# Kernel optimization log

Hardware: AMD Instinct MI355X
Metric: run time of the kernel (lower is better)

## Reference

```python
import jax, jax.numpy as jnp
import numpy as np
from jax import lax

P = 16        # patch spatial size (C = 3 * P * P = 768)
CH = 3        # channels per patch
H = 8         # num attention heads
EPS_BN = 1e-3 # keras BatchNormalization default epsilon
EPS_LN = 1e-3 # keras LayerNormalization default epsilon


def _layernorm(x, g, b):
    mu = jnp.mean(x, axis=-1, keepdims=True)
    var = jnp.mean(jnp.square(x - mu), axis=-1, keepdims=True)
    return (x - mu) * lax.rsqrt(var + EPS_LN) * g + b


def setup_inputs() -> dict:
    key = jax.random.key(0)
    ks = jax.random.split(key, 8)
    B, N, C, DFF = 8, 1024, 768, 3072
    s = 0.02
    return {
        "encoded_patches": jax.random.normal(ks[0], (B, N, C), jnp.float32),
        "qconv_w": jax.random.normal(ks[1], (3, 3, CH, CH), jnp.float32) * 0.2,
        "reatten_w": jax.random.normal(ks[2], (H, H), jnp.float32) * 0.3,
        "reatten_b": jnp.zeros((H,), jnp.float32),
        "bn_gamma": jnp.ones((H,), jnp.float32),
        "bn_beta": jnp.zeros((H,), jnp.float32),
        "proj_w": jax.random.normal(ks[3], (C, C), jnp.float32) * s,
        "proj_b": jnp.zeros((C,), jnp.float32),
        "ffn_w1": jax.random.normal(ks[4], (C, DFF), jnp.float32) * s,
        "ffn_b1": jnp.zeros((DFF,), jnp.float32),
        "ffn_w2": jax.random.normal(ks[5], (DFF, C), jnp.float32) * s,
        "ffn_b2": jnp.zeros((C,), jnp.float32),
        "ln1_g": jnp.ones((C,), jnp.float32),
        "ln1_b": jnp.zeros((C,), jnp.float32),
        "ln2_g": jnp.ones((C,), jnp.float32),
        "ln2_b": jnp.zeros((C,), jnp.float32),
    }


def reference(encoded_patches, qconv_w, reatten_w, reatten_b, bn_gamma, bn_beta,
              proj_w, proj_b, ffn_w1, ffn_b1, ffn_w2, ffn_b2,
              ln1_g, ln1_b, ln2_g, ln2_b):
    B, N, C = encoded_patches.shape
    hd = C // H
    scale = jnp.float32(hd) ** -0.5

    # create_queries: unflatten [B,N,C] -> [B*N,P,P,CH], 3x3 'same' conv,
    # flatten back and split heads -> [B,H,N,hd]. Source uses qconv2d for
    # q, k AND v, so q == k == v; compute once.
    y = encoded_patches.reshape(B * N, P, P, CH)
    y = lax.conv_general_dilated(y, qconv_w, (1, 1), 'SAME',
                                 dimension_numbers=('NHWC', 'HWIO', 'NHWC'))
    q = y.reshape(B, N, H, hd).transpose(0, 2, 1, 3)  # [B,H,N,hd]
    k = q
    v = q

    # attention scores + softmax: [B,H,N,N]
    attn = jax.nn.softmax(jnp.einsum('bhnd,bhmd->bhnm', q, k) * scale, axis=-1)

    # re-attention: 1x1 conv mixing heads + BatchNorm (inference: mean=0, var=1)
    attn = jnp.einsum('bhnm,gh->bgnm', attn, reatten_w) + reatten_b[None, :, None, None]
    bn_s = bn_gamma * lax.rsqrt(jnp.float32(1.0) + EPS_BN)
    attn = attn * bn_s[None, :, None, None] + bn_beta[None, :, None, None]
    # reatten_scale = 1.0 (transform_scale=False)

    x = jnp.einsum('bhnm,bhmd->bhnd', attn, v)        # [B,H,N,hd]
    x = x.transpose(0, 2, 1, 3).reshape(B, N, C)
    x = x @ proj_w + proj_b

    x = x + encoded_patches          # residual
    x = _layernorm(x, ln1_g, ln1_b)  # LN1

    h = jax.nn.gelu(x @ ffn_w1 + ffn_b1, approximate=False)
    x = (h @ ffn_w2 + ffn_b2) + x    # FFN + residual
    x = _layernorm(x, ln2_g, ln2_b)  # LN2
    return x
```

## Files before the change

kernel.cpp:

```cpp
#include <hip/hip_runtime.h>
#include <hip/hip_bf16.h>
#include <math.h>

#define B_ 8
#define N_ 1024
#define C_ 768
#define H_ 8
#define HD_ 96
#define DFF_ 3072
#define SC2_ 0.14724454f
#define SH2_ 11.5415602f

typedef __attribute__((ext_vector_type(8))) short bf16x8;
typedef __attribute__((ext_vector_type(4))) float f32x4;
typedef __attribute__((ext_vector_type(4))) short sh4;

__device__ __forceinline__ short f2bf(float f){
  __hip_bfloat16 h = __float2bfloat16(f);
  return __builtin_bit_cast(short, h);
}
__device__ __forceinline__ float bf2f(short s){
  unsigned u = ((unsigned)(unsigned short)s) << 16;
  return __builtin_bit_cast(float, u);
}
#define MFMA16(a,b,c) __builtin_amdgcn_mfma_f32_16x16x32_bf16((a),(b),(c),0,0,0)

__device__ __forceinline__ void gload16(const void* g, void* l){
  __builtin_amdgcn_global_load_lds((const __attribute__((address_space(1))) unsigned int*)g,
                                   (__attribute__((address_space(3))) unsigned int*)l, 16, 0, 0);
}

__global__ void conv_q_kernel(const float* __restrict__ x, const float* __restrict__ w,
                              short* __restrict__ qb){
  int p = blockIdx.x;
  int t = threadIdx.x;
  __shared__ float xs[768];
  __shared__ float ws[81];
  const float* xp = x + (size_t)p * 768;
  xs[t] = xp[t]; xs[t+256] = xp[t+256]; xs[t+512] = xp[t+512];
  if (t < 81) ws[t] = w[t];
  __syncthreads();
  int i = t >> 4, j = t & 15;
  float a0=0.f, a1=0.f, a2=0.f;
  #pragma unroll
  for (int di=0; di<3; ++di){
    int ii = i + di - 1;
    if (ii < 0 || ii > 15) continue;
    #pragma unroll
    for (int dj=0; dj<3; ++dj){
      int jj = j + dj - 1;
      if (jj < 0 || jj > 15) continue;
      const float* cell = &xs[(ii*16+jj)*3];
      const float* wp = &ws[(di*3+dj)*9];
      #pragma unroll
      for (int ci=0; ci<3; ++ci){
        float xv = cell[ci];
        a0 += xv * wp[ci*3+0];
        a1 += xv * wp[ci*3+1];
        a2 += xv * wp[ci*3+2];
      }
    }
  }
  short* qp = qb + (size_t)p*768 + t*3;
  qp[0]=f2bf(a0); qp[1]=f2bf(a1); qp[2]=f2bf(a2);
}

__global__ void vt_kernel(const short* __restrict__ in, short* __restrict__ out){
  __shared__ short tile[32][33];
  int b = blockIdx.z;
  int c0 = blockIdx.x*32, n0 = blockIdx.y*32;
  int t = threadIdx.x;
  const short* ib = in + (size_t)b*N_*C_;
  short* ob = out + (size_t)b*C_*N_;
  #pragma unroll
  for (int i=0;i<4;i++){
    int idx = i*256+t; int r = idx>>5, cc = idx&31;
    tile[r][cc] = ib[(size_t)(n0+r)*C_ + c0+cc];
  }
  __syncthreads();
  #pragma unroll
  for (int i=0;i<4;i++){
    int idx = i*256+t; int r = idx>>5, cc = idx&31;
    ob[(size_t)(c0+r)*N_ + n0+cc] = tile[cc][r];
  }
}

__global__ void wtrans_kernel(const float* __restrict__ in, short* __restrict__ out,
                              int K, int Nn){
  __shared__ float tile[32][33];
  int n0 = blockIdx.x*32, k0 = blockIdx.y*32;
  int t = threadIdx.x;
  #pragma unroll
  for (int i=0;i<4;i++){
    int idx=i*256+t; int r=idx>>5, cc=idx&31;
    tile[r][cc] = in[(size_t)(k0+r)*Nn + n0+cc];
  }
  __syncthreads();
  #pragma unroll
  for (int i=0;i<4;i++){
    int idx=i*256+t; int r=idx>>5, cc=idx&31;
    out[(size_t)(n0+r)*K + k0+cc] = f2bf(tile[cc][r]);
  }
}

__global__ __launch_bounds__(256, 2)
void qkexp_kernel(const short* __restrict__ qb, short* __restrict__ Pt,
                  float* __restrict__ lsums, int b0)
{
  __shared__ short Ks[64*104];
  int bid = blockIdx.x;
  int bhl = bid >> 4, nt = bid & 15;
  int b = b0 + (bhl >> 3), h = bhl & 7;
  int n0 = nt*64;
  int t = threadIdx.x, w = t>>6, l = t&63, lg = l>>4, lr = l&15;
  const short* qbase = qb + (size_t)b*N_*C_;

  bf16x8 qf[3];
  #pragma unroll
  for (int kc=0;kc<3;++kc)
    qf[kc] = *(const bf16x8*)(qbase + (size_t)(n0 + w*16 + lr)*C_ + h*HD_ + kc*32 + lg*8);

  bf16x8 kreg[3];
  #pragma unroll
  for (int i=0;i<3;++i){
    int id = i*256+t; int r = id/12, c = id%12;
    kreg[i] = *(const bf16x8*)(qbase + (size_t)r*C_ + h*HD_ + c*8);
  }

  float lsum = 0.f;
  short* prow = Pt + ((size_t)bhl*1024 + n0 + w*16 + lr)*1024;

  for (int mt=0; mt<16; ++mt){
    int m0 = mt*64;
    __syncthreads();
    #pragma unroll
    for (int i=0;i<3;++i){
      int id = i*256+t; int r = id/12, c = id%12;
      *(bf16x8*)&Ks[r*104 + c*8] = kreg[i];
    }
    __syncthreads();
    if (mt < 15){
      int m1 = m0 + 64;
      #pragma unroll
      for (int i=0;i<3;++i){
        int id = i*256+t; int r = id/12, c = id%12;
        kreg[i] = *(const bf16x8*)(qbase + (size_t)(m1+r)*C_ + h*HD_ + c*8);
      }
    }
    #pragma unroll
    for (int s=0;s<4;++s){
      f32x4 sacc = (f32x4){0.f,0.f,0.f,0.f};
      bf16x8 kf[3];
      #pragma unroll
      for (int kc=0;kc<3;++kc)
        kf[kc] = *(const bf16x8*)&Ks[(s*16+lr)*104 + kc*32 + lg*8];
      #pragma unroll
      for (int kc=0;kc<3;++kc)
        sacc = MFMA16(kf[kc], qf[kc], sacc);
      sh4 pv;
      #pragma unroll
      for (int r=0;r<4;++r){
        float e = exp2f(sacc[r]*SC2_ - SH2_);
        lsum += e;
        pv[r] = f2bf(e);
      }
      *(sh4*)&prow[m0 + s*16 + lg*4] = pv;
    }
  }
  lsum += __shfl_xor(lsum, 16);
  lsum += __shfl_xor(lsum, 32);
  if (l < 16) lsums[(size_t)bhl*1024 + n0 + w*16 + l] = lsum;
}

__device__ __forceinline__ void load_mix(const short* __restrict__ Pt, int b_local,
                                         int n0, int m0, int t,
                                         const float wl[4][8], float cw, bf16x8 amc[4]){
  #pragma unroll
  for (int i=0;i<4;++i){
    int r = i*32 + (t>>3), mo = t&7;
    const short* p0 = Pt + ((size_t)(b_local*8)*1024 + (size_t)(n0+r))*1024 + m0 + mo*8;
    float pm[8];
    #pragma unroll
    for (int j=0;j<8;++j) pm[j] = cw;
    #pragma unroll
    for (int h=0;h<8;++h){
      bf16x8 ph = *(const bf16x8*)(p0 + (size_t)h*1024*1024);
      #pragma unroll
      for (int j=0;j<8;++j) pm[j] += wl[i][h]*bf2f(ph[j]);
    }
    #pragma unroll
    for (int j=0;j<8;++j) amc[i][j] = f2bf(pm[j]);
  }
}

__global__ __launch_bounds__(256, 2)
void mixpv_kernel(const short* __restrict__ Pt, const float* __restrict__ lsums,
                  const short* __restrict__ vt, const float* __restrict__ rw,
                  const float* __restrict__ rb, const float* __restrict__ bng,
                  const float* __restrict__ bnb, short* __restrict__ out, int b0)
{
  __shared__ short Am[128*68];
  int bid = blockIdx.x;
  int rank = bid>>3;
  int g = rank & 7;
  int p = (bid&7) + ((rank>>3)<<3);
  int b_local = p>>3;
  int n0 = (p&7)*128;
  int b = b0 + b_local;
  int t = threadIdx.x, w = t>>6, l = t&63, lg = l>>4, lr = l&15;

  float bns = bng[g]*rsqrtf(1.001f);
  float cw = rb[g]*bns + bnb[g];
  float wl[4][8];
  #pragma unroll
  for (int i=0;i<4;++i){
    int r = i*32 + (t>>3);
    #pragma unroll
    for (int h=0;h<8;++h)
      wl[i][h] = (rw[g*8+h]*bns) / lsums[(size_t)(b_local*8+h)*1024 + n0 + r];
  }

  f32x4 acc[2][6];
  #pragma unroll
  for (int a=0;a<2;++a)
    #pragma unroll
    for (int nt=0;nt<6;++nt) acc[a][nt] = (f32x4){0.f,0.f,0.f,0.f};

  bf16x8 amc[4];
  load_mix(Pt, b_local, n0, 0, t, wl, cw, amc);
  const short* vbase = vt + (size_t)b*C_*N_ + (size_t)g*HD_*N_;

  for (int mt=0; mt<16; ++mt){
    int m0 = mt*64;
    __syncthreads();
    #pragma unroll
    for (int i=0;i<4;++i){
      int r = i*32 + (t>>3), mo = t&7;
      *(bf16x8*)&Am[r*68 + mo*8] = amc[i];
    }
    __syncthreads();
    if (mt < 15) load_mix(Pt, b_local, n0, m0+64, t, wl, cw, amc);
    #pragma unroll
    for (int kc=0;kc<2;++kc){
      bf16x8 af[2], bfr[6];
      #pragma unroll
      for (int a=0;a<2;++a)
        af[a] = *(const bf16x8*)&Am[(w*32 + a*16 + lr)*68 + kc*32 + lg*8];
      #pragma unroll
      for (int nt=0;nt<6;++nt)
        bfr[nt] = *(const bf16x8*)(vbase + (size_t)(nt*16+lr)*N_ + m0 + kc*32 + lg*8);
      #pragma unroll
      for (int a=0;a<2;++a)
        #pragma unroll
        for (int nt=0;nt<6;++nt)
          acc[a][nt] = MFMA16(af[a], bfr[nt], acc[a][nt]);
    }
  }

  short* obase = out + (size_t)b*N_*C_;
  #pragma unroll
  for (int a=0;a<2;++a)
    #pragma unroll
    for (int nt=0;nt<6;++nt)
      #pragma unroll
      for (int r=0;r<4;++r)
        obase[(size_t)(n0 + w*32 + a*16 + lg*4 + r)*C_ + g*HD_ + nt*16 + lr]
            = f2bf(acc[a][nt][r]);
}

template<int EPI>
__global__ __launch_bounds__(256, 2)
void gemm_bt_kernel(const short* __restrict__ A, const short* __restrict__ Bt,
                    const float* __restrict__ bias, const float* __restrict__ res,
                    float* __restrict__ Of, short* __restrict__ Ob,
                    int M, int Nn, int K)
{
  __shared__ __align__(16) char smem[65536];
  short* Sb = (short*)smem;
  int gm = blockIdx.y*128, gn = blockIdx.x*128;
  int tid = threadIdx.x;
  int w = tid>>6, l = tid&63, lg = l>>4, lr = l&15;
  int wr = w>>1, wc = w&1;
  int srow = l>>3;
  int sg = (l&7) ^ srow;

  const short* Ap = A  + (size_t)(gm + w*8 + srow)*K + sg*8;
  const short* Bp = Bt + (size_t)(gn + w*8 + srow)*K + sg*8;

  f32x4 acc[4][4];
  #pragma unroll
  for (int mt=0;mt<4;++mt)
    #pragma unroll
    for (int nt=0;nt<4;++nt) acc[mt][nt] = (f32x4){0.f,0.f,0.f,0.f};

  int nk = K >> 6;

  {
    short* dA = Sb; short* dB = Sb + 8192;
    #pragma unroll
    for (int j=0;j<4;++j){
      gload16(Ap + (size_t)j*32*K, dA + (j*32 + w*8)*64);
      gload16(Bp + (size_t)j*32*K, dB + (j*32 + w*8)*64);
    }
  }
  asm volatile("s_waitcnt vmcnt(0)" ::: "memory");
  __syncthreads();

  int cur = 0;
  for (int t=0; t<nk; ++t){
    if (t+1 < nk){
      short* dA = Sb + (cur^1)*16384;
      short* dB = dA + 8192;
      int kb = (t+1)<<6;
      #pragma unroll
      for (int j=0;j<4;++j){
        gload16(Ap + (size_t)j*32*K + kb, dA + (j*32 + w*8)*64);
        gload16(Bp + (size_t)j*32*K + kb, dB + (j*32 + w*8)*64);
      }
    }
    short* CA = Sb + cur*16384;
    short* CB = CA + 8192;
    #pragma unroll
    for (int kc=0;kc<2;++kc){
      bf16x8 af[4], bfr[4];
      #pragma unroll
      for (int mt=0;mt<4;++mt){
        int row = wr*64+mt*16+lr;
        af[mt] = *(const bf16x8*)&CA[row*64 + (((kc*4+lg)^(lr&7))*8)];
      }
      #pragma unroll
      for (int nt=0;nt<4;++nt){
        int row = wc*64+nt*16+lr;
        bfr[nt] = *(const bf16x8*)&CB[row*64 + (((kc*4+lg)^(lr&7))*8)];
      }
      #pragma unroll
      for (int mt=0;mt<4;++mt)
        #pragma unroll
        for (int nt=0;nt<4;++nt)
          acc[mt][nt] = MFMA16(af[mt], bfr[nt], acc[mt][nt]);
    }
    asm volatile("s_waitcnt vmcnt(0)" ::: "memory");
    __syncthreads();
    cur ^= 1;
  }

  float* Cl = (float*)smem;
  #pragma unroll
  for (int mt=0;mt<4;++mt)
    #pragma unroll
    for (int nt=0;nt<4;++nt)
      #pragma unroll
      for (int r=0;r<4;++r){
        int row = wr*64 + mt*16 + lg*4 + r;
        int col = wc*64 + nt*16 + lr;
        Cl[row*128 + (col ^ ((row&7)<<2))] = acc[mt][nt][r];
      }
  __syncthreads();
  #pragma unroll
  for (int seg=0; seg<16; ++seg){
    int row = seg*8 + (tid>>5);
    int col = (tid&31)*4;
    int colp = col ^ ((row&7)<<2);
    f32x4 c = *(f32x4*)&Cl[row*128 + colp];
    float4 bi = *(const float4*)&bias[gn+col];
    size_t goff = (size_t)(gm+row)*Nn + gn + col;
    if (EPI == 0){
      float4 rs = *(const float4*)&res[goff];
      float4 o = { c[0]+bi.x+rs.x, c[1]+bi.y+rs.y, c[2]+bi.z+rs.z, c[3]+bi.w+rs.w };
      *(float4*)&Of[goff] = o;
    } else {
      float v0 = c[0]+bi.x, v1 = c[1]+bi.y, v2 = c[2]+bi.z, v3 = c[3]+bi.w;
      v0 = 0.5f*v0*(1.0f + erff(v0*0.70710678118654752f));
      v1 = 0.5f*v1*(1.0f + erff(v1*0.70710678118654752f));
      v2 = 0.5f*v2*(1.0f + erff(v2*0.70710678118654752f));
      v3 = 0.5f*v3*(1.0f + erff(v3*0.70710678118654752f));
      sh4 ob = { f2bf(v0), f2bf(v1), f2bf(v2), f2bf(v3) };
      *(sh4*)&Ob[goff] = ob;
    }
  }
}

template<int WB>
__global__ void ln_kernel(const float* __restrict__ in, const float* __restrict__ gam,
                          const float* __restrict__ bet, float* __restrict__ of,
                          short* __restrict__ ob)
{
  int row = blockIdx.x*4 + (threadIdx.x>>6);
  int l = threadIdx.x & 63;
  const float* ip = in + (size_t)row*C_;
  float v[12];
  #pragma unroll
  for (int i=0;i<3;i++) *(float4*)&v[i*4] = *(const float4*)(ip + i*256 + l*4);
  float s = 0.f;
  #pragma unroll
  for (int i=0;i<12;i++) s += v[i];
  #pragma unroll
  for (int off=1; off<64; off<<=1) s += __shfl_xor(s, off);
  float mu = s * (1.0f/768.0f);
  float q = 0.f;
  #pragma unroll
  for (int i=0;i<12;i++){ float d = v[i]-mu; q += d*d; }
  #pragma unroll
  for (int off=1; off<64; off<<=1) q += __shfl_xor(q, off);
  float rstd = rsqrtf(q*(1.0f/768.0f) + 1e-3f);
  #pragma unroll
  for (int i=0;i<3;i++){
    float4 gv = *(const float4*)(gam + i*256 + l*4);
    float4 bv = *(const float4*)(bet + i*256 + l*4);
    float o0 = (v[i*4+0]-mu)*rstd*gv.x + bv.x;
    float o1 = (v[i*4+1]-mu)*rstd*gv.y + bv.y;
    float o2 = (v[i*4+2]-mu)*rstd*gv.z + bv.z;
    float o3 = (v[i*4+3]-mu)*rstd*gv.w + bv.w;
    float4 ov = {o0,o1,o2,o3};
    *(float4*)(of + (size_t)row*C_ + i*256 + l*4) = ov;
    if (WB){
      sh4 obv = { f2bf(o0), f2bf(o1), f2bf(o2), f2bf(o3) };
      *(sh4*)(ob + (size_t)row*C_ + i*256 + l*4) = obv;
    }
  }
}

extern "C" void kernel_launch(void* const* d_in, const int* in_sizes, int n_in,
                              void* d_out, int out_size, void* d_ws, size_t ws_size,
                              hipStream_t stream)
{
  const float* enc       = (const float*)d_in[0];
  const float* qconv_w   = (const float*)d_in[1];
  const float* reatten_w = (const float*)d_in[2];
  const float* reatten_b = (const float*)d_in[3];
  const float* bn_gamma  = (const float*)d_in[4];
  const float* bn_beta   = (const float*)d_in[5];
  const float* proj_w    = (const float*)d_in[6];
  const float* proj_b    = (const float*)d_in[7];
  const float* ffn_w1    = (const float*)d_in[8];
  const float* ffn_b1    = (const float*)d_in[9];
  const float* ffn_w2    = (const float*)d_in[10];
  const float* ffn_b2    = (const float*)d_in[11];
  const float* ln1_g     = (const float*)d_in[12];
  const float* ln1_b     = (const float*)d_in[13];
  const float* ln2_g     = (const float*)d_in[14];
  const float* ln2_b     = (const float*)d_in[15];
  float* outp = (float*)d_out;

  char* ws = (char*)d_ws;
  short* qbuf  = (short*)(ws);
  short* vtbuf = (short*)(ws + 12582912);
  short* atbuf = (short*)(ws + 25165824);
  short* ptbuf = (short*)(ws + 37748736);
  float* lsums = (float*)(ws + 104857600);
  float* ypre  = (float*)(ws + 37748736);
  float* x1    = (float*)(ws + 62914560);
  short* x1b   = (short*)(ws + 88080384);
  short* hbuf  = (short*)(ws + 100663296);
  short* wpt   = (short*)(ws + 150994944);
  short* w1t   = (short*)(ws + 152174592);
  short* w2t   = (short*)(ws + 156893184);

  conv_q_kernel<<<B_*N_, 256, 0, stream>>>(enc, qconv_w, qbuf);
  vt_kernel<<<dim3(C_/32, N_/32, B_), 256, 0, stream>>>(qbuf, vtbuf);
  wtrans_kernel<<<dim3(C_/32,  C_/32), 256, 0, stream>>>(proj_w, wpt, C_,  C_);
  wtrans_kernel<<<dim3(DFF_/32, C_/32), 256, 0, stream>>>(ffn_w1, w1t, C_,  DFF_);
  wtrans_kernel<<<dim3(C_/32, DFF_/32), 256, 0, stream>>>(ffn_w2, w2t, DFF_, C_);

  for (int half=0; half<2; ++half){
    int b0 = half*4;
    qkexp_kernel<<<512, 256, 0, stream>>>(qbuf, ptbuf, lsums, b0);
    mixpv_kernel<<<256, 256, 0, stream>>>(ptbuf, lsums, vtbuf, reatten_w, reatten_b,
                                          bn_gamma, bn_beta, atbuf, b0);
  }

  gemm_bt_kernel<0><<<dim3(C_/128, (B_*N_)/128), 256, 0, stream>>>(
      atbuf, wpt, proj_b, enc, ypre, nullptr, B_*N_, C_, C_);
  ln_kernel<1><<<(B_*N_)/4, 256, 0, stream>>>(ypre, ln1_g, ln1_b, x1, x1b);
  gemm_bt_kernel<1><<<dim3(DFF_/128, (B_*N_)/128), 256, 0, stream>>>(
      x1b, w1t, ffn_b1, nullptr, nullptr, hbuf, B_*N_, DFF_, C_);
  gemm_bt_kernel<0><<<dim3(C_/128, (B_*N_)/128), 256, 0, stream>>>(
      hbuf, w2t, ffn_b2, x1, ypre, nullptr, B_*N_, C_, DFF_);
  ln_kernel<0><<<(B_*N_)/4, 256, 0, stream>>>(ypre, ln2_g, ln2_b, outp, nullptr);
}
```

Baseline: 387.0 us.

## Prefetch two K-stages ahead in GEMM with partial vmcnt waits

Restructures the GEMM main loop so two stages of global-to-LDS loads are in flight: the prologue issues stages 0 and 1, and each iteration waits only until the current stage has landed (vmcnt(8)) before computing. After the MFMAs it waits on LDS reads, barriers, and issues stage t+2 into the freed buffer. This is meant to hide more global load latency behind compute, at the cost of an extra barrier per iteration and reliance on exact vmcnt accounting.

```diff
diff --git a/kernel.cpp b/kernel.cpp
--- a/kernel.cpp
+++ b/kernel.cpp
@@ -295,30 +295,25 @@
 
   int nk = K >> 6;
 
-  {
-    short* dA = Sb; short* dB = Sb + 8192;
+  auto stage = [&](int tt){
+    short* dA = Sb + (tt&1)*16384;
+    short* dB = dA + 8192;
+    int kb = tt<<6;
     #pragma unroll
     for (int j=0;j<4;++j){
-      gload16(Ap + (size_t)j*32*K, dA + (j*32 + w*8)*64);
-      gload16(Bp + (size_t)j*32*K, dB + (j*32 + w*8)*64);
-    }
-  }
-  asm volatile("s_waitcnt vmcnt(0)" ::: "memory");
-  __syncthreads();
-
-  int cur = 0;
+      gload16(Ap + (size_t)j*32*K + kb, dA + (j*32 + w*8)*64);
+      gload16(Bp + (size_t)j*32*K + kb, dB + (j*32 + w*8)*64);
+    }
+  };
+
+  stage(0);
+  if (nk > 1) stage(1);
+
   for (int t=0; t<nk; ++t){
-    if (t+1 < nk){
-      short* dA = Sb + (cur^1)*16384;
-      short* dB = dA + 8192;
-      int kb = (t+1)<<6;
-      #pragma unroll
-      for (int j=0;j<4;++j){
-        gload16(Ap + (size_t)j*32*K + kb, dA + (j*32 + w*8)*64);
-        gload16(Bp + (size_t)j*32*K + kb, dB + (j*32 + w*8)*64);
-      }
-    }
-    short* CA = Sb + cur*16384;
+    if (t < nk-1) asm volatile("s_waitcnt vmcnt(8)" ::: "memory");
+    else          asm volatile("s_waitcnt vmcnt(0)" ::: "memory");
+    __builtin_amdgcn_s_barrier();
+    short* CA = Sb + (t&1)*16384;
     short* CB = CA + 8192;
     #pragma unroll
     for (int kc=0;kc<2;++kc){
@@ -339,11 +334,13 @@
         for (int nt=0;nt<4;++nt)
           acc[mt][nt] = MFMA16(af[mt], bfr[nt], acc[mt][nt]);
     }
-    asm volatile("s_waitcnt vmcnt(0)" ::: "memory");
-    __syncthreads();
-    cur ^= 1;
-  }
-
+    asm volatile("s_waitcnt lgkmcnt(0)" ::: "memory");
+    __builtin_amdgcn_sched_barrier(0);
+    __builtin_amdgcn_s_barrier();
+    if (t+2 < nk) stage(t+2);
+  }
+
+  __builtin_amdgcn_s_barrier();
   float* Cl = (float*)smem;
   #pragma unroll
   for (int mt=0;mt<4;++mt)
```

Measured after the change: 390.3 us (median of 2 runs). About the same (+0.9%).
